# Kernel tuning notes

Hardware: AMD Instinct MI355X
Metric: run time of the kernel (lower is better)

## Reference

```python
import jax, jax.numpy as jnp
import numpy as np

N = 50000
E = 800000
HID = 128
OUT = 64
HEADS = 4
NEG_SLOPE = 0.2


def gat_layer(x, edge_index, W, att_src, att_dst, bias):
    """PyG-style GATConv: shared linear for src/dst, additive attention,
    self-loops, segment softmax over incoming edges, concat heads + bias."""
    n = x.shape[0]
    H, C = att_src.shape
    # add self loops (PyG default add_self_loops=True)
    loops = jnp.arange(n, dtype=edge_index.dtype)
    src = jnp.concatenate([edge_index[0], loops])  # message sources j
    dst = jnp.concatenate([edge_index[1], loops])  # aggregation targets i
    xl = (x @ W).reshape(n, H, C)                  # [N,H,C]
    a_s = jnp.einsum('nhc,hc->nh', xl, att_src)    # [N,H]
    a_d = jnp.einsum('nhc,hc->nh', xl, att_dst)    # [N,H]
    e = jax.nn.leaky_relu(a_s[src] + a_d[dst], NEG_SLOPE)   # [E',H]
    m = jax.ops.segment_max(e, dst, num_segments=n)         # stable softmax
    e = jnp.exp(e - m[dst])
    denom = jax.ops.segment_sum(e, dst, num_segments=n)
    alpha = e / (denom[dst] + 1e-16)                        # [E',H]
    msg = xl[src] * alpha[:, :, None]                       # [E',H,C]
    out = jax.ops.segment_sum(msg, dst, num_segments=n)     # [N,H,C]
    return out.reshape(n, H * C) + bias


def setup_inputs() -> dict:
    key = jax.random.key(0)
    ks = jax.random.split(key, 16)
    C = HID // HEADS  # per-head channels = 32
    x = jax.random.normal(ks[0], (N, HID), dtype=jnp.float32)
    edge_indices = jax.random.randint(ks[1], (3, 2, E), 0, N, dtype=jnp.int32)
    s = 0.1
    inp = {
        'x': x,
        'edge_indices': edge_indices,
        'W1': jax.random.normal(ks[2], (HID, HEADS * C), dtype=jnp.float32) * s,
        'as1': jax.random.normal(ks[3], (HEADS, C), dtype=jnp.float32) * s,
        'ad1': jax.random.normal(ks[4], (HEADS, C), dtype=jnp.float32) * s,
        'b1': jnp.zeros((HEADS * C,), dtype=jnp.float32),
        'W2': jax.random.normal(ks[5], (HID, HEADS * C), dtype=jnp.float32) * s,
        'as2': jax.random.normal(ks[6], (HEADS, C), dtype=jnp.float32) * s,
        'ad2': jax.random.normal(ks[7], (HEADS, C), dtype=jnp.float32) * s,
        'b2': jnp.zeros((HEADS * C,), dtype=jnp.float32),
        'W3': jax.random.normal(ks[8], (HID, OUT), dtype=jnp.float32) * s,
        'as3': jax.random.normal(ks[9], (1, OUT), dtype=jnp.float32) * s,
        'ad3': jax.random.normal(ks[10], (1, OUT), dtype=jnp.float32) * s,
        'b3': jnp.zeros((OUT,), dtype=jnp.float32),
    }
    return inp


def reference(x, edge_indices, W1, as1, ad1, b1, W2, as2, ad2, b2, W3, as3, ad3, b3):
    h = jax.nn.relu(gat_layer(x, edge_indices[0], W1, as1, ad1, b1))
    h = jax.nn.relu(gat_layer(h, edge_indices[1], W2, as2, ad2, b2))
    out = gat_layer(h, edge_indices[2], W3, as3, ad3, b3)  # no ReLU on last layer
    return out
```

## Files before the change

kernel.cpp:

```cpp
#include <hip/hip_runtime.h>

typedef unsigned short u16;
typedef unsigned int u32;

#define HID 128

static inline int cdiv(long long a, int b) { return (int)((a + b - 1) / b); }

__device__ __forceinline__ float bfbits(u32 u) { union { u32 u; float f; } c; c.u = u; return c.f; }
__device__ __forceinline__ u16 f2bf(float f) {
  union { float f; u32 u; } c; c.f = f;
  u32 u = c.u;
  return (u16)((u + 0x7fffu + ((u >> 16) & 1u)) >> 16);
}
__device__ __forceinline__ u32 pack2bf(float a, float b) {
  return (u32)f2bf(a) | ((u32)f2bf(b) << 16);
}

template <int COUT, int HEADS>
__global__ __launch_bounds__(256) void gemm_attn(
    const float* __restrict__ Hin, const float* __restrict__ W,
    const float* __restrict__ attS, const float* __restrict__ attD,
    u16* __restrict__ XL, float* __restrict__ aS, float* __restrict__ aD, int n) {
  constexpr int RT = 4;
  constexpr int TN = COUT / 8;
  constexpr int TM = 256 / TN;
  constexpr int MT = TM * RT;
  constexpr int HALF = COUT / 2;
  constexpr int C = COUT / HEADS;
  constexpr bool SAMEHEAD = (HALF < C);

  __shared__ float xs[32][MT + 4];
  __shared__ float ws[32][COUT];

  int t = threadIdx.x;
  int tx = t % TN, ty = t / TN;
  int rowBase = blockIdx.x * MT;

  float acc[RT][8];
#pragma unroll
  for (int r = 0; r < RT; ++r)
#pragma unroll
    for (int c = 0; c < 8; ++c) acc[r][c] = 0.f;

  for (int kb = 0; kb < 4; ++kb) {
    __syncthreads();
    {
      int kg = (t & 7) * 4;
#pragma unroll
      for (int pass = 0; pass < MT / 32; ++pass) {
        int rr = pass * 32 + (t >> 3);
        int grow = rowBase + rr;
        float4 v = make_float4(0.f, 0.f, 0.f, 0.f);
        if (grow < n) v = *(const float4*)(Hin + (size_t)grow * HID + kb * 32 + kg);
        xs[kg + 0][rr] = v.x;
        xs[kg + 1][rr] = v.y;
        xs[kg + 2][rr] = v.z;
        xs[kg + 3][rr] = v.w;
      }
    }
    {
      constexpr int WF = 32 * COUT / 256;
      const float* wp = W + (size_t)kb * 32 * COUT;
      float* wsf = &ws[0][0];
#pragma unroll
      for (int u = 0; u < WF; u += 4) {
        int idx = t * WF + u;
        *(float4*)(wsf + idx) = *(const float4*)(wp + idx);
      }
    }
    __syncthreads();
#pragma unroll 8
    for (int k = 0; k < 32; ++k) {
      const float4 xv0 = *(const float4*)&xs[k][ty * RT];
      const float4 wv0 = *(const float4*)&ws[k][tx * 4];
      const float4 wv1 = *(const float4*)&ws[k][HALF + tx * 4];
      const float xr[RT] = {xv0.x, xv0.y, xv0.z, xv0.w};
      const float wc[8] = {wv0.x, wv0.y, wv0.z, wv0.w, wv1.x, wv1.y, wv1.z, wv1.w};
#pragma unroll
      for (int r = 0; r < RT; ++r)
#pragma unroll
        for (int c = 0; c < 8; ++c) acc[r][c] += xr[r] * wc[c];
    }
  }

  float sv[8], dv[8];
#pragma unroll
  for (int j = 0; j < 4; ++j) {
    sv[j] = attS[tx * 4 + j];
    sv[4 + j] = attS[HALF + tx * 4 + j];
    dv[j] = attD[tx * 4 + j];
    dv[4 + j] = attD[HALF + tx * 4 + j];
  }
  int row0 = rowBase + ty * RT;
  int hlo = (tx * 4) / C;
  int hhi = (HALF + tx * 4) / C;
  u32* XLo = (u32*)XL;
#pragma unroll
  for (int r = 0; r < RT; ++r) {
    int row = row0 + r;
    bool ok = (row < n);
    if (ok) {
      u32 lo01 = pack2bf(acc[r][0], acc[r][1]);
      u32 lo23 = pack2bf(acc[r][2], acc[r][3]);
      u32 hi01 = pack2bf(acc[r][4], acc[r][5]);
      u32 hi23 = pack2bf(acc[r][6], acc[r][7]);
      *(uint2*)(XLo + (size_t)row * (COUT / 2) + tx * 2) = make_uint2(lo01, lo23);
      *(uint2*)(XLo + (size_t)row * (COUT / 2) + COUT / 4 + tx * 2) = make_uint2(hi01, hi23);
    }
    float pslo = acc[r][0] * sv[0] + acc[r][1] * sv[1] + acc[r][2] * sv[2] + acc[r][3] * sv[3];
    float pshi = acc[r][4] * sv[4] + acc[r][5] * sv[5] + acc[r][6] * sv[6] + acc[r][7] * sv[7];
    float pdlo = acc[r][0] * dv[0] + acc[r][1] * dv[1] + acc[r][2] * dv[2] + acc[r][3] * dv[3];
    float pdhi = acc[r][4] * dv[4] + acc[r][5] * dv[5] + acc[r][6] * dv[6] + acc[r][7] * dv[7];
    if (SAMEHEAD) { pslo += pshi; pdlo += pdhi; }
#pragma unroll
    for (int mk = 1; mk < 8; mk <<= 1) {
      pslo += __shfl_xor(pslo, mk);
      pdlo += __shfl_xor(pdlo, mk);
      if (!SAMEHEAD) {
        pshi += __shfl_xor(pshi, mk);
        pdhi += __shfl_xor(pdhi, mk);
      }
    }
    if (((tx & 7) == 0) && ok) {
      aS[(size_t)row * HEADS + hlo] = pslo;
      aD[(size_t)row * HEADS + hlo] = pdlo;
      if (!SAMEHEAD) {
        aS[(size_t)row * HEADS + hhi] = pshi;
        aD[(size_t)row * HEADS + hhi] = pdhi;
      }
    }
  }
}

#define PSTR 16

__global__ __launch_bounds__(256) void bucket_hist(const int* __restrict__ ei,
                                                   int* __restrict__ cntP,
                                                   int e4, int rem, int E, int NB) {
  int L = blockIdx.y;
  const int* dst = ei + (size_t)(2 * L + 1) * E;
  __shared__ int cnt[256];
  int t = threadIdx.x;
  cnt[t] = 0;
  __syncthreads();
  int gbase = blockIdx.x * 1024 + t;
#pragma unroll
  for (int u = 0; u < 4; ++u) {
    int g = gbase + u * 256;
    if (g < e4) {
      int4 d = *(const int4*)(dst + g * 4);
      atomicAdd(&cnt[d.x >> 8], 1);
      atomicAdd(&cnt[d.y >> 8], 1);
      atomicAdd(&cnt[d.z >> 8], 1);
      atomicAdd(&cnt[d.w >> 8], 1);
    }
  }
  if (blockIdx.x == 0 && t < rem) atomicAdd(&cnt[dst[e4 * 4 + t] >> 8], 1);
  __syncthreads();
  int c = cnt[t];
  if (t < NB && c > 0) atomicAdd(&cntP[(L * NB + t) * PSTR], c);
}

__global__ __launch_bounds__(256) void bucket_scan(const int* __restrict__ cntP,
                                                   int* __restrict__ bucketOff,
                                                   int* __restrict__ curP, int NB, int E) {
  int L = blockIdx.x;
  int t = threadIdx.x;
  int lane = t & 63, wid = t >> 6;
  __shared__ int wpart[4];
  int v = (t < NB) ? cntP[(L * NB + t) * PSTR] : 0;
  int inc = v;
#pragma unroll
  for (int off = 1; off < 64; off <<= 1) {
    int w = __shfl_up(inc, (unsigned)off, 64);
    if (lane >= off) inc += w;
  }
  if (lane == 63) wpart[wid] = inc;
  __syncthreads();
  if (t == 0) {
    int a = 0;
#pragma unroll
    for (int k = 0; k < 4; ++k) { int tmp = wpart[k]; wpart[k] = a; a += tmp; }
  }
  __syncthreads();
  int ex = wpart[wid] + inc - v;
  if (t < NB) {
    bucketOff[L * (NB + 1) + t] = ex;
    curP[(L * NB + t) * PSTR] = ex;
  }
  if (t == 0) bucketOff[L * (NB + 1) + NB] = E;
}

__global__ __launch_bounds__(256) void bucket_scatter(const int* __restrict__ ei,
                                                      int* __restrict__ curP,
                                                      int2* __restrict__ pairsAll,
                                                      int e4, int rem, int E, int NB) {
  int L = blockIdx.y;
  const int* src = ei + (size_t)(2 * L) * E;
  const int* dst = src + E;
  int2* pairs = pairsAll + (size_t)L * E;
  __shared__ int cnt[256];
  __shared__ int baseS[256];
  int t = threadIdx.x;
  cnt[t] = 0;
  __syncthreads();

  int gbase = blockIdx.x * 1024 + t;
  int4 dv[4], sv[4];
  bool val[4];
#pragma unroll
  for (int u = 0; u < 4; ++u) {
    int g = gbase + u * 256;
    val[u] = (g < e4);
    if (val[u]) {
      dv[u] = *(const int4*)(dst + g * 4);
      sv[u] = *(const int4*)(src + g * 4);
      atomicAdd(&cnt[dv[u].x >> 8], 1);
      atomicAdd(&cnt[dv[u].y >> 8], 1);
      atomicAdd(&cnt[dv[u].z >> 8], 1);
      atomicAdd(&cnt[dv[u].w >> 8], 1);
    }
  }
  int tailS = 0, tailD = 0;
  bool hasTail = (blockIdx.x == 0 && t < rem);
  if (hasTail) {
    tailD = dst[e4 * 4 + t];
    tailS = src[e4 * 4 + t];
    atomicAdd(&cnt[tailD >> 8], 1);
  }
  __syncthreads();
  int c = cnt[t];
  if (t < NB && c > 0) baseS[t] = atomicAdd(&curP[(L * NB + t) * PSTR], c);
  __syncthreads();
  cnt[t] = 0;
  __syncthreads();
#pragma unroll
  for (int u = 0; u < 4; ++u) {
    if (val[u]) {
      int b, p;
      b = dv[u].x >> 8; p = atomicAdd(&cnt[b], 1); pairs[baseS[b] + p] = make_int2(sv[u].x, dv[u].x);
      b = dv[u].y >> 8; p = atomicAdd(&cnt[b], 1); pairs[baseS[b] + p] = make_int2(sv[u].y, dv[u].y);
      b = dv[u].z >> 8; p = atomicAdd(&cnt[b], 1); pairs[baseS[b] + p] = make_int2(sv[u].z, dv[u].z);
      b = dv[u].w >> 8; p = atomicAdd(&cnt[b], 1); pairs[baseS[b] + p] = make_int2(sv[u].w, dv[u].w);
    }
  }
  if (hasTail) {
    int b = tailD >> 8;
    int p = atomicAdd(&cnt[b], 1);
    pairs[baseS[b] + p] = make_int2(tailS, tailD);
  }
}

__global__ __launch_bounds__(256) void csr_finalize(const int2* __restrict__ pairsAll,
                                                    const int* __restrict__ bucketOff,
                                                    int* __restrict__ indptrAll,
                                                    int* __restrict__ srcIdxAll,
                                                    int N, int E, int NB) {
  int L = blockIdx.y, b = blockIdx.x;
  const int2* pairs = pairsAll + (size_t)L * E;
  int* indptr = indptrAll + (size_t)L * (N + 1);
  int* srcL = srcIdxAll + (size_t)L * (E + N);
  int base = b << 8;
  int nodes = min(256, N - base);
  int p0 = bucketOff[L * (NB + 1) + b];
  int p1 = bucketOff[L * (NB + 1) + b + 1];

  __shared__ int cnt[256];
  __shared__ int wpart[4];
  int t = threadIdx.x;
  int lane = t & 63, wid = t >> 6;
  cnt[t] = 0;
  __syncthreads();

  for (int i = p0 + t; i < p1; i += 256) atomicAdd(&cnt[pairs[i].y - base], 1);
  __syncthreads();

  int v = (t < nodes) ? cnt[t] + 1 : 0;
  int inc = v;
#pragma unroll
  for (int off = 1; off < 64; off <<= 1) {
    int w = __shfl_up(inc, (unsigned)off, 64);
    if (lane >= off) inc += w;
  }
  if (lane == 63) wpart[wid] = inc;
  __syncthreads();
  if (t == 0) {
    int a = 0;
#pragma unroll
    for (int k = 0; k < 4; ++k) { int tmp = wpart[k]; wpart[k] = a; a += tmp; }
  }
  __syncthreads();
  int ex = wpart[wid] + inc - v;
  __syncthreads();
  if (t < nodes) {
    int segStart = p0 + base + ex;
    indptr[base + t] = segStart;
    srcL[segStart] = base + t;
    cnt[t] = segStart + 1;
  }
  if (b == NB - 1 && t == 0) indptr[N] = E + N;
  __syncthreads();

  for (int i = p0 + t; i < p1; i += 256) {
    int2 pr = pairs[i];
    int p = atomicAdd(&cnt[pr.y - base], 1);
    srcL[p] = pr.x;
  }
}

template <int COUT, int HEADS, bool RELU>
__global__ __launch_bounds__(256) void aggregate(
    const u16* __restrict__ XL, const float* __restrict__ aS, const float* __restrict__ aD,
    const int* __restrict__ indptr, const int* __restrict__ srcIdx,
    const float* __restrict__ bias, float* __restrict__ outF, int n) {
  constexpr int VPL = 8;
  constexpr int LPG = COUT / VPL;
  constexpr int G = 64 / LPG;
  constexpr int C = COUT / HEADS;
  int wave = (blockIdx.x * blockDim.x + threadIdx.x) >> 6;
  if (wave >= n) return;
  int lane = threadIdx.x & 63;
  int g = lane / LPG;
  int cl = lane % LPG;
  int col0 = cl * VPL;
  int h = col0 / C;
  int i = wave;
  float ad = aD[i * HEADS + h];
  float s = 0.f;
  float acc[VPL];
#pragma unroll
  for (int v = 0; v < VPL; ++v) acc[v] = 0.f;
  int e0 = indptr[i], e1 = indptr[i + 1];
  const u32* XL32 = (const u32*)XL;

  auto doEdge = [&](int loadIdx, bool act) {
    int j = srcIdx[loadIdx];
    float a = aS[j * HEADS + h];
    uint4 px = *(const uint4*)(XL32 + j * (COUT / 2) + cl * 4);
    float l = a + ad;
    l = (l >= 0.f) ? l : 0.2f * l;
    float el = act ? __expf(fminf(l, 60.f)) : 0.f;
    s += el;
    acc[0] += el * bfbits(px.x << 16);
    acc[1] += el * bfbits(px.x & 0xffff0000u);
    acc[2] += el * bfbits(px.y << 16);
    acc[3] += el * bfbits(px.y & 0xffff0000u);
    acc[4] += el * bfbits(px.z << 16);
    acc[5] += el * bfbits(px.z & 0xffff0000u);
    acc[6] += el * bfbits(px.w << 16);
    acc[7] += el * bfbits(px.w & 0xffff0000u);
  };

  int idx = e0;
  for (; idx + 2 * G <= e1; idx += 2 * G) {
    doEdge(idx + g, true);
    doEdge(idx + G + g, true);
  }
  for (; idx + G <= e1; idx += G) doEdge(idx + g, true);
  int r = e1 - idx;
  if (r > 0) doEdge((g < r) ? (idx + g) : e0, g < r);

#pragma unroll
  for (int mk = LPG; mk < 64; mk <<= 1) {
    s += __shfl_xor(s, mk);
#pragma unroll
    for (int v = 0; v < VPL; ++v) acc[v] += __shfl_xor(acc[v], mk);
  }

  if (g == 0) {
    float inv = 1.f / (s + 1e-16f);
    float o[VPL];
#pragma unroll
    for (int v = 0; v < VPL; ++v) {
      o[v] = acc[v] * inv + bias[col0 + v];
      if (RELU) o[v] = fmaxf(o[v], 0.f);
    }
    float* op = outF + (size_t)i * COUT + col0;
    *(float4*)op = make_float4(o[0], o[1], o[2], o[3]);
    *(float4*)(op + 4) = make_float4(o[4], o[5], o[6], o[7]);
  }
}

extern "C" void kernel_launch(void* const* d_in, const int* in_sizes, int n_in,
                              void* d_out, int out_size, void* d_ws, size_t ws_size,
                              hipStream_t stream) {
  const float* x = (const float*)d_in[0];
  const int* ei = (const int*)d_in[1];
  const float* W1 = (const float*)d_in[2];
  const float* as1 = (const float*)d_in[3];
  const float* ad1 = (const float*)d_in[4];
  const float* b1 = (const float*)d_in[5];
  const float* W2 = (const float*)d_in[6];
  const float* as2 = (const float*)d_in[7];
  const float* ad2 = (const float*)d_in[8];
  const float* b2 = (const float*)d_in[9];
  const float* W3 = (const float*)d_in[10];
  const float* as3 = (const float*)d_in[11];
  const float* ad3 = (const float*)d_in[12];
  const float* b3 = (const float*)d_in[13];

  int N = in_sizes[0] / HID;
  int E = in_sizes[1] / 6;
  int NB = cdiv(N, 256);

  char* w = (char*)d_ws;
  auto alloc = [&](size_t bytes) {
    void* q = (void*)w;
    w += (bytes + 255) & ~(size_t)255;
    return q;
  };
  float* bufH = (float*)alloc((size_t)N * HID * 4);
  u16* bufXL = (u16*)alloc((size_t)N * HID * 2);
  float* aS = (float*)alloc((size_t)N * 4 * 4);
  float* aD = (float*)alloc((size_t)N * 4 * 4);
  int* cntP = (int*)alloc((size_t)3 * NB * PSTR * 4);
  int* curP = (int*)alloc((size_t)3 * NB * PSTR * 4);
  int* bucketOff = (int*)alloc((size_t)3 * (NB + 1) * 4);
  int2* pairsAll = (int2*)alloc((size_t)3 * E * 8);
  int* indptrAll = (int*)alloc((size_t)3 * (N + 1) * 4);
  int* srcIdxAll = (int*)alloc((size_t)3 * (E + N) * 4);

  int e4 = E >> 2, rem = E & 3;
  int gx = cdiv(e4, 1024);

  hipMemsetAsync(cntP, 0, (size_t)3 * NB * PSTR * 4, stream);
  {
    dim3 g(gx, 3);
    bucket_hist<<<g, 256, 0, stream>>>(ei, cntP, e4, rem, E, NB);
  }
  bucket_scan<<<3, 256, 0, stream>>>(cntP, bucketOff, curP, NB, E);
  {
    dim3 g(gx, 3);
    bucket_scatter<<<g, 256, 0, stream>>>(ei, curP, pairsAll, e4, rem, E, NB);
  }
  {
    dim3 g(NB, 3);
    csr_finalize<<<g, 256, 0, stream>>>(pairsAll, bucketOff, indptrAll, srcIdxAll, N, E, NB);
  }

  gemm_attn<128, 4><<<cdiv(N, 64), 256, 0, stream>>>(x, W1, as1, ad1, bufXL, aS, aD, N);
  aggregate<128, 4, true><<<cdiv(N, 4), 256, 0, stream>>>(
      bufXL, aS, aD, indptrAll, srcIdxAll, b1, bufH, N);
  gemm_attn<128, 4><<<cdiv(N, 64), 256, 0, stream>>>(bufH, W2, as2, ad2, bufXL, aS, aD, N);
  aggregate<128, 4, true><<<cdiv(N, 4), 256, 0, stream>>>(
      bufXL, aS, aD, indptrAll + (N + 1), srcIdxAll + (size_t)(E + N), b2, bufH, N);
  gemm_attn<64, 1><<<cdiv(N, 128), 256, 0, stream>>>(bufH, W3, as3, ad3, bufXL, aS, aD, N);
  aggregate<64, 1, false><<<cdiv(N, 4), 256, 0, stream>>>(
      bufXL, aS, aD, indptrAll + 2 * (N + 1), srcIdxAll + (size_t)2 * (E + N), b3,
      (float*)d_out, N);
}
```

Measured before the change: 341.8 us.

## Use bf16 MFMA for node linear transform with pre-transposed bf16 weights

Replaces the FP32 register-tiled SIMT GEMM with a bf16 MFMA 16x16x32 kernel. Input rows are converted to bf16 in shared memory and the weights are transposed and converted to bf16 by a new small prep kernel. The attention projections are computed from the MFMA accumulators with cross-lane shuffles. The aim is to cut the GEMM compute time, at the cost of bf16 rounding of the inputs and weights and three extra tiny kernel launches.

```diff
diff --git a/kernel.cpp b/kernel.cpp
--- a/kernel.cpp
+++ b/kernel.cpp
@@ -2,6 +2,8 @@
 
 typedef unsigned short u16;
 typedef unsigned int u32;
+typedef __attribute__((ext_vector_type(8))) short short8;
+typedef __attribute__((ext_vector_type(4))) float f32x4;
 
 #define HID 128
 
@@ -17,118 +19,98 @@
   return (u32)f2bf(a) | ((u32)f2bf(b) << 16);
 }
 
+__global__ __launch_bounds__(256) void prep_wt(const float* __restrict__ W,
+                                               u16* __restrict__ WT, int cout) {
+  int idx = blockIdx.x * 256 + threadIdx.x;
+  if (idx < 128 * cout) {
+    int k = idx / cout, c = idx - k * cout;
+    WT[c * 128 + k] = f2bf(W[idx]);
+  }
+}
+
 template <int COUT, int HEADS>
-__global__ __launch_bounds__(256) void gemm_attn(
-    const float* __restrict__ Hin, const float* __restrict__ W,
+__global__ __launch_bounds__(256) void gemm_attn_mfma(
+    const float* __restrict__ Hin, const u16* __restrict__ WT,
     const float* __restrict__ attS, const float* __restrict__ attD,
     u16* __restrict__ XL, float* __restrict__ aS, float* __restrict__ aD, int n) {
-  constexpr int RT = 4;
-  constexpr int TN = COUT / 8;
-  constexpr int TM = 256 / TN;
-  constexpr int MT = TM * RT;
-  constexpr int HALF = COUT / 2;
+  constexpr int BM = 64;
+  constexpr int NT = COUT / 16;
   constexpr int C = COUT / HEADS;
-  constexpr bool SAMEHEAD = (HALF < C);
-
-  __shared__ float xs[32][MT + 4];
-  __shared__ float ws[32][COUT];
+  constexpr int TPH = C / 16;
+
+  __shared__ u16 aT[BM][136];
 
   int t = threadIdx.x;
-  int tx = t % TN, ty = t / TN;
-  int rowBase = blockIdx.x * MT;
-
-  float acc[RT][8];
-#pragma unroll
-  for (int r = 0; r < RT; ++r)
-#pragma unroll
-    for (int c = 0; c < 8; ++c) acc[r][c] = 0.f;
-
+  int rowBase = blockIdx.x * BM;
+
+#pragma unroll
+  for (int p = 0; p < 8; ++p) {
+    int id = p * 256 + t;
+    int r = id >> 5;
+    int c4 = id & 31;
+    int grow = rowBase + r;
+    float4 v = make_float4(0.f, 0.f, 0.f, 0.f);
+    if (grow < n) v = *(const float4*)(Hin + (size_t)grow * HID + c4 * 4);
+    *(uint2*)&aT[r][c4 * 4] = make_uint2(pack2bf(v.x, v.y), pack2bf(v.z, v.w));
+  }
+  __syncthreads();
+
+  int wv = t >> 6;
+  int ln = t & 63;
+  int lrow = ln & 15;
+  int lk = ln >> 4;
+
+  f32x4 acc[NT];
+#pragma unroll
+  for (int ct = 0; ct < NT; ++ct) acc[ct] = {0.f, 0.f, 0.f, 0.f};
+
+#pragma unroll
   for (int kb = 0; kb < 4; ++kb) {
-    __syncthreads();
-    {
-      int kg = (t & 7) * 4;
-#pragma unroll
-      for (int pass = 0; pass < MT / 32; ++pass) {
-        int rr = pass * 32 + (t >> 3);
-        int grow = rowBase + rr;
-        float4 v = make_float4(0.f, 0.f, 0.f, 0.f);
-        if (grow < n) v = *(const float4*)(Hin + (size_t)grow * HID + kb * 32 + kg);
-        xs[kg + 0][rr] = v.x;
-        xs[kg + 1][rr] = v.y;
-        xs[kg + 2][rr] = v.z;
-        xs[kg + 3][rr] = v.w;
-      }
-    }
-    {
-      constexpr int WF = 32 * COUT / 256;
-      const float* wp = W + (size_t)kb * 32 * COUT;
-      float* wsf = &ws[0][0];
-#pragma unroll
-      for (int u = 0; u < WF; u += 4) {
-        int idx = t * WF + u;
-        *(float4*)(wsf + idx) = *(const float4*)(wp + idx);
-      }
-    }
-    __syncthreads();
-#pragma unroll 8
-    for (int k = 0; k < 32; ++k) {
-      const float4 xv0 = *(const float4*)&xs[k][ty * RT];
-      const float4 wv0 = *(const float4*)&ws[k][tx * 4];
-      const float4 wv1 = *(const float4*)&ws[k][HALF + tx * 4];
-      const float xr[RT] = {xv0.x, xv0.y, xv0.z, xv0.w};
-      const float wc[8] = {wv0.x, wv0.y, wv0.z, wv0.w, wv1.x, wv1.y, wv1.z, wv1.w};
-#pragma unroll
-      for (int r = 0; r < RT; ++r)
-#pragma unroll
-        for (int c = 0; c < 8; ++c) acc[r][c] += xr[r] * wc[c];
-    }
-  }
-
-  float sv[8], dv[8];
-#pragma unroll
-  for (int j = 0; j < 4; ++j) {
-    sv[j] = attS[tx * 4 + j];
-    sv[4 + j] = attS[HALF + tx * 4 + j];
-    dv[j] = attD[tx * 4 + j];
-    dv[4 + j] = attD[HALF + tx * 4 + j];
-  }
-  int row0 = rowBase + ty * RT;
-  int hlo = (tx * 4) / C;
-  int hhi = (HALF + tx * 4) / C;
-  u32* XLo = (u32*)XL;
-#pragma unroll
-  for (int r = 0; r < RT; ++r) {
-    int row = row0 + r;
-    bool ok = (row < n);
-    if (ok) {
-      u32 lo01 = pack2bf(acc[r][0], acc[r][1]);
-      u32 lo23 = pack2bf(acc[r][2], acc[r][3]);
-      u32 hi01 = pack2bf(acc[r][4], acc[r][5]);
-      u32 hi23 = pack2bf(acc[r][6], acc[r][7]);
-      *(uint2*)(XLo + (size_t)row * (COUT / 2) + tx * 2) = make_uint2(lo01, lo23);
-      *(uint2*)(XLo + (size_t)row * (COUT / 2) + COUT / 4 + tx * 2) = make_uint2(hi01, hi23);
-    }
-    float pslo = acc[r][0] * sv[0] + acc[r][1] * sv[1] + acc[r][2] * sv[2] + acc[r][3] * sv[3];
-    float pshi = acc[r][4] * sv[4] + acc[r][5] * sv[5] + acc[r][6] * sv[6] + acc[r][7] * sv[7];
-    float pdlo = acc[r][0] * dv[0] + acc[r][1] * dv[1] + acc[r][2] * dv[2] + acc[r][3] * dv[3];
-    float pdhi = acc[r][4] * dv[4] + acc[r][5] * dv[5] + acc[r][6] * dv[6] + acc[r][7] * dv[7];
-    if (SAMEHEAD) { pslo += pshi; pdlo += pdhi; }
-#pragma unroll
-    for (int mk = 1; mk < 8; mk <<= 1) {
-      pslo += __shfl_xor(pslo, mk);
-      pdlo += __shfl_xor(pdlo, mk);
-      if (!SAMEHEAD) {
-        pshi += __shfl_xor(pshi, mk);
-        pdhi += __shfl_xor(pdhi, mk);
-      }
-    }
-    if (((tx & 7) == 0) && ok) {
-      aS[(size_t)row * HEADS + hlo] = pslo;
-      aD[(size_t)row * HEADS + hlo] = pdlo;
-      if (!SAMEHEAD) {
-        aS[(size_t)row * HEADS + hhi] = pshi;
-        aD[(size_t)row * HEADS + hhi] = pdhi;
-      }
+    short8 bh = *(const short8*)&aT[wv * 16 + lrow][kb * 32 + lk * 8];
+    const u16* wp = WT + (size_t)lrow * HID + kb * 32 + lk * 8;
+#pragma unroll
+    for (int ct = 0; ct < NT; ++ct) {
+      short8 aw = *(const short8*)(wp + (size_t)ct * 16 * HID);
+      acc[ct] = __builtin_amdgcn_mfma_f32_16x16x32_bf16(aw, bh, acc[ct], 0, 0, 0);
+    }
+  }
+
+  int row = rowBase + wv * 16 + lrow;
+
+  float pS[HEADS], pD[HEADS];
+#pragma unroll
+  for (int h = 0; h < HEADS; ++h) { pS[h] = 0.f; pD[h] = 0.f; }
+#pragma unroll
+  for (int ct = 0; ct < NT; ++ct) {
+    float4 sv = *(const float4*)(attS + ct * 16 + lk * 4);
+    float4 dv = *(const float4*)(attD + ct * 16 + lk * 4);
+    int h = ct / TPH;
+    pS[h] += acc[ct][0] * sv.x + acc[ct][1] * sv.y + acc[ct][2] * sv.z + acc[ct][3] * sv.w;
+    pD[h] += acc[ct][0] * dv.x + acc[ct][1] * dv.y + acc[ct][2] * dv.z + acc[ct][3] * dv.w;
+  }
+#pragma unroll
+  for (int h = 0; h < HEADS; ++h) {
+    pS[h] += __shfl_xor(pS[h], 16);
+    pS[h] += __shfl_xor(pS[h], 32);
+    pD[h] += __shfl_xor(pD[h], 16);
+    pD[h] += __shfl_xor(pD[h], 32);
+  }
+  if (lk == 0 && row < n) {
+    if (HEADS == 4) {
+      *(float4*)(aS + (size_t)row * 4) = make_float4(pS[0], pS[1], pS[2], pS[3]);
+      *(float4*)(aD + (size_t)row * 4) = make_float4(pD[0], pD[1], pD[2], pD[3]);
+    } else {
+      aS[row] = pS[0];
+      aD[row] = pD[0];
+    }
+  }
+
+  if (row < n) {
+    u32* Xp = (u32*)XL + (size_t)row * (COUT / 2);
+#pragma unroll
+    for (int ct = 0; ct < NT; ++ct) {
+      *(uint2*)(Xp + ct * 8 + lk * 2) =
+          make_uint2(pack2bf(acc[ct][0], acc[ct][1]), pack2bf(acc[ct][2], acc[ct][3]));
     }
   }
 }
@@ -414,6 +396,9 @@
   u16* bufXL = (u16*)alloc((size_t)N * HID * 2);
   float* aS = (float*)alloc((size_t)N * 4 * 4);
   float* aD = (float*)alloc((size_t)N * 4 * 4);
+  u16* wt1 = (u16*)alloc((size_t)128 * 128 * 2);
+  u16* wt2 = (u16*)alloc((size_t)128 * 128 * 2);
+  u16* wt3 = (u16*)alloc((size_t)64 * 128 * 2);
   int* cntP = (int*)alloc((size_t)3 * NB * PSTR * 4);
   int* curP = (int*)alloc((size_t)3 * NB * PSTR * 4);
   int* bucketOff = (int*)alloc((size_t)3 * (NB + 1) * 4);
@@ -424,6 +409,10 @@
   int e4 = E >> 2, rem = E & 3;
   int gx = cdiv(e4, 1024);
 
+  prep_wt<<<64, 256, 0, stream>>>(W1, wt1, 128);
+  prep_wt<<<64, 256, 0, stream>>>(W2, wt2, 128);
+  prep_wt<<<32, 256, 0, stream>>>(W3, wt3, 64);
+
   hipMemsetAsync(cntP, 0, (size_t)3 * NB * PSTR * 4, stream);
   {
     dim3 g(gx, 3);
@@ -439,13 +428,13 @@
     csr_finalize<<<g, 256, 0, stream>>>(pairsAll, bucketOff, indptrAll, srcIdxAll, N, E, NB);
   }
 
-  gemm_attn<128, 4><<<cdiv(N, 64), 256, 0, stream>>>(x, W1, as1, ad1, bufXL, aS, aD, N);
+  gemm_attn_mfma<128, 4><<<cdiv(N, 64), 256, 0, stream>>>(x, wt1, as1, ad1, bufXL, aS, aD, N);
   aggregate<128, 4, true><<<cdiv(N, 4), 256, 0, stream>>>(
       bufXL, aS, aD, indptrAll, srcIdxAll, b1, bufH, N);
-  gemm_attn<128, 4><<<cdiv(N, 64), 256, 0, stream>>>(bufH, W2, as2, ad2, bufXL, aS, aD, N);
+  gemm_attn_mfma<128, 4><<<cdiv(N, 64), 256, 0, stream>>>(bufH, wt2, as2, ad2, bufXL, aS, aD, N);
   aggregate<128, 4, true><<<cdiv(N, 4), 256, 0, stream>>>(
       bufXL, aS, aD, indptrAll + (N + 1), srcIdxAll + (size_t)(E + N), b2, bufH, N);
-  gemm_attn<64, 1><<<cdiv(N, 128), 256, 0, stream>>>(bufH, W3, as3, ad3, bufXL, aS, aD, N);
+  gemm_attn_mfma<64, 1><<<cdiv(N, 64), 256, 0, stream>>>(bufH, wt3, as3, ad3, bufXL, aS, aD, N);
   aggregate<64, 1, false><<<cdiv(N, 4), 256, 0, stream>>>(
       bufXL, aS, aD, indptrAll + 2 * (N + 1), srcIdxAll + (size_t)2 * (E + N), b3,
       (float*)d_out, N);
```

After: 325.0 us. 1.05x faster.
